# Kernel tuning notes

Measured on AMD Instinct MI355X. Metric: run time of the kernel, lower is better.

Reference implementation:

```python
import jax, jax.numpy as jnp
import numpy as np

N, E, H, XD, ED, YD, L = 10000, 640000, 128, 8, 8, 112, 4
EPS_MSG = 1e-7   # GENConv message eps
EPS_SM = 1e-16   # pyg softmax denom eps
EPS_LN = 1e-5    # layernorm eps


def node_ln(x, g, b):
    # torch.nn.LayerNorm over last dim
    m = x.mean(axis=-1, keepdims=True)
    v = x.var(axis=-1, keepdims=True)
    return (x - m) * jax.lax.rsqrt(v + EPS_LN) * g + b


def graph_ln(x, g, b):
    # pyg LayerNorm mode='graph' (no batch): global mean/std over all nodes+channels
    xc = x - x.mean()
    std = jnp.sqrt((xc * xc).mean())
    return xc / (std + EPS_LN) * g + b


def setup_inputs() -> dict:
    key = jax.random.key(0)
    ks = jax.random.split(key, 10)
    rn = lambda k, s, sc: jax.random.normal(k, s, jnp.float32) * sc
    return {
        "x": jax.random.normal(ks[0], (N, XD), jnp.float32),
        "edge_index": jax.random.randint(ks[1], (2, E), 0, N),
        "edge_attr": jax.random.normal(ks[2], (E, ED), jnp.float32),
        "Wn": rn(ks[3], (XD, H), 0.3), "bn": jnp.zeros((H,), jnp.float32),
        "We": rn(ks[4], (ED, H), 0.3), "be": jnp.zeros((H,), jnp.float32),
        "t": jnp.ones((L,), jnp.float32),
        "W1": rn(ks[5], (L, H, 2 * H), 0.08), "b1": jnp.zeros((L, 2 * H), jnp.float32),
        "g1": jnp.ones((L, 2 * H), jnp.float32), "bt1": jnp.zeros((L, 2 * H), jnp.float32),
        "W2": rn(ks[6], (L, 2 * H, H), 0.08), "b2": jnp.zeros((L, H), jnp.float32),
        "lng": jnp.ones((L, H), jnp.float32), "lnb": jnp.zeros((L, H), jnp.float32),
        "Wout": rn(ks[7], (H, YD), 0.08), "bout": jnp.zeros((YD,), jnp.float32),
    }


def reference(x, edge_index, edge_attr, Wn, bn, We, be, t, W1, b1, g1, bt1,
              W2, b2, lng, lnb, Wout, bout):
    src, dst = edge_index[0], edge_index[1]
    h = x @ Wn + bn                       # [N,H] node encoder
    ea = edge_attr @ We + be              # [E,H] edge encoder

    def gen_conv(h, i):
        msg = jax.nn.relu(h[src] + ea) + EPS_MSG          # [E,H]
        logit = msg * t[i]
        mx = jax.ops.segment_max(logit, dst, num_segments=N)
        ex = jnp.exp(logit - mx[dst])
        den = jax.ops.segment_sum(ex, dst, num_segments=N)
        alpha = ex / (den[dst] + EPS_SM)
        agg = jax.ops.segment_sum(alpha * msg, dst, num_segments=N) + h  # root add
        z = jax.nn.relu(graph_ln(agg @ W1[i] + b1[i], g1[i], bt1[i]))
        return z @ W2[i] + b2[i]

    h = gen_conv(h, 0)                    # first layer: conv only
    for i in range(1, L):                 # res+ blocks (dropout off: eval)
        r = jax.nn.relu(node_ln(h, lng[i], lnb[i]))
        h = h + gen_conv(r, i)
    h = jax.nn.relu(node_ln(h, lng[0], lnb[0]))  # layers[0].act(layers[0].norm(x))
    return h @ Wout + bout
```

## Files before the change

### kernel.cpp

```cpp
#include <hip/hip_runtime.h>
#include <math.h>

#define NN 10000
#define NE 640000
#define H 128
#define H2 256
#define XD 8
#define ED 8
#define YD 112
#define NL 4
#define EPS_MSG 1e-7f
#define EPS_SM 1e-16f
#define EPS_LN 1e-5f
#define TM 8
#define NB1 (NN / TM)
#define TNO 16
#define NBO (NN / TNO)

typedef _Float16 h2 __attribute__((ext_vector_type(2)));

__global__ void hist_k(const int* __restrict__ dst, int* __restrict__ counts) {
    int e = blockIdx.x * 256 + threadIdx.x;
    if (e < NE) atomicAdd(&counts[dst[e]], 1);
}

__global__ void scan_k(const int* __restrict__ counts, int* __restrict__ rowptr) {
    __shared__ int part[1024];
    int tid = threadIdx.x;
    const int CH = (NN + 1023) / 1024;
    int base = tid * CH;
    int s = 0;
    for (int j = 0; j < CH; j++) { int i = base + j; if (i < NN) s += counts[i]; }
    part[tid] = s; __syncthreads();
    for (int off = 1; off < 1024; off <<= 1) {
        int v = (tid >= off) ? part[tid - off] : 0;
        __syncthreads();
        part[tid] += v;
        __syncthreads();
    }
    int run = part[tid] - s;
    for (int j = 0; j < CH; j++) {
        int i = base + j;
        if (i < NN) { rowptr[i] = run; run += counts[i]; }
    }
    if (tid == 1023) rowptr[NN] = run;
}

__global__ void scatter_k(const int* __restrict__ dst, const int* __restrict__ rowptr,
                          int* __restrict__ fill, int* __restrict__ perm) {
    int e = blockIdx.x * 256 + threadIdx.x;
    if (e >= NE) return;
    int d = dst[e];
    int pos = rowptr[d] + atomicAdd(&fill[d], 1);
    perm[pos] = e;
}

__global__ void __launch_bounds__(256) packenc_k(
    const int* __restrict__ perm, const int* __restrict__ src,
    const float* __restrict__ eattr, int* __restrict__ srcs,
    _Float16* __restrict__ eacsr,
    const float* __restrict__ x, const float* __restrict__ Wn,
    const float* __restrict__ bn, float* __restrict__ h,
    _Float16* __restrict__ rh16) {
    int b = blockIdx.x;
    if (b < 2500) {
        int pos = b * 256 + threadIdx.x;
        int e = perm[pos];
        srcs[pos] = src[e];
        const float4* ein = (const float4*)eattr;
        float4 a = ein[(size_t)e * 2];
        float4 bb = ein[(size_t)e * 2 + 1];
        float4 pk;
        _Float16* pp = (_Float16*)&pk;
        pp[0] = (_Float16)a.x; pp[1] = (_Float16)a.y; pp[2] = (_Float16)a.z; pp[3] = (_Float16)a.w;
        pp[4] = (_Float16)bb.x; pp[5] = (_Float16)bb.y; pp[6] = (_Float16)bb.z; pp[7] = (_Float16)bb.w;
        ((float4*)eacsr)[pos] = pk;
    } else {
        int bb = b - 2500;
        int c = threadIdx.x & 127, ln = threadIdx.x >> 7;
        int n = bb * 2 + ln;
        const float4* xr = (const float4*)(x + (size_t)n * XD);
        float4 x0 = xr[0], x1 = xr[1];
        float acc = bn[c];
        acc = fmaf(x0.x, Wn[0 * H + c], acc); acc = fmaf(x0.y, Wn[1 * H + c], acc);
        acc = fmaf(x0.z, Wn[2 * H + c], acc); acc = fmaf(x0.w, Wn[3 * H + c], acc);
        acc = fmaf(x1.x, Wn[4 * H + c], acc); acc = fmaf(x1.y, Wn[5 * H + c], acc);
        acc = fmaf(x1.z, Wn[6 * H + c], acc); acc = fmaf(x1.w, Wn[7 * H + c], acc);
        h[(size_t)n * H + c] = acc;
        rh16[(size_t)n * H + c] = (_Float16)acc;
    }
}

__global__ void __launch_bounds__(512) ea_mm1_k(
    const float* __restrict__ rin, const _Float16* __restrict__ rh16,
    const int* __restrict__ rowptr,
    const int* __restrict__ srcs, const _Float16* __restrict__ eacsr,
    const float* __restrict__ We, const float* __restrict__ be,
    const float* __restrict__ tptr, int layer,
    const float* __restrict__ W1i, const float* __restrict__ b1i,
    float* __restrict__ y1, float* __restrict__ part) {
    int nb = blockIdx.x, tid = threadIdx.x;
    int n0 = nb * TM;
    __shared__ float a[TM][H];

    {
        int wv = tid >> 6, l = tid & 63;
        int c0 = 2 * l;
        int n = n0 + wv;
        h2 wA[4], wB[4];
#pragma unroll
        for (int k = 0; k < 4; k++) {
            wA[k][0] = (_Float16)We[(2 * k) * H + c0];
            wA[k][1] = (_Float16)We[(2 * k + 1) * H + c0];
            wB[k][0] = (_Float16)We[(2 * k) * H + c0 + 1];
            wB[k][1] = (_Float16)We[(2 * k + 1) * H + c0 + 1];
        }
        float becA = be[c0], becB = be[c0 + 1];
        float ts2 = tptr[layer] * 1.44269504088896f;
        int beg = __builtin_amdgcn_readfirstlane(rowptr[n]);
        int end = __builtin_amdgcn_readfirstlane(rowptr[n + 1]);
        const float2 rv = *(const float2*)(rin + (size_t)n * H + c0);
        float denA = 0.f, numA = 0.f, denB = 0.f, numB = 0.f;
#pragma unroll 4
        for (int j = beg; j < end; ++j) {
            int sn = srcs[j];
            float4 raw = *(const float4*)(eacsr + (size_t)j * ED);
            const h2* ep = (const h2*)&raw;
            h2 hv2 = *(const h2*)(rh16 + (size_t)sn * H + c0);
            float hvA = (float)hv2[0], hvB = (float)hv2[1];
            float pA = __builtin_amdgcn_fdot2(ep[0], wA[0], becA, false);
            pA = __builtin_amdgcn_fdot2(ep[1], wA[1], pA, false);
            pA = __builtin_amdgcn_fdot2(ep[2], wA[2], pA, false);
            pA = __builtin_amdgcn_fdot2(ep[3], wA[3], pA, false);
            float pB = __builtin_amdgcn_fdot2(ep[0], wB[0], becB, false);
            pB = __builtin_amdgcn_fdot2(ep[1], wB[1], pB, false);
            pB = __builtin_amdgcn_fdot2(ep[2], wB[2], pB, false);
            pB = __builtin_amdgcn_fdot2(ep[3], wB[3], pB, false);
            float msgA = fmaxf(hvA + pA, 0.f) + EPS_MSG;
            float msgB = fmaxf(hvB + pB, 0.f) + EPS_MSG;
            float peA = __builtin_amdgcn_exp2f(msgA * ts2);
            float peB = __builtin_amdgcn_exp2f(msgB * ts2);
            denA += peA; numA = fmaf(peA, msgA, numA);
            denB += peB; numB = fmaf(peB, msgB, numB);
        }
        float2 av;
        av.x = numA / (denA + EPS_SM) + rv.x;
        av.y = numB / (denB + EPS_SM) + rv.y;
        *(float2*)&a[wv][c0] = av;
    }
    __syncthreads();

    int o = tid & 255, half = tid >> 8;
    int rb = half * 4;
    float acc[4];
#pragma unroll
    for (int i = 0; i < 4; i++) acc[i] = 0.f;
    for (int k = 0; k < H; k += 4) {
        float w0 = W1i[k * H2 + o];
        float w1 = W1i[(k + 1) * H2 + o];
        float w2 = W1i[(k + 2) * H2 + o];
        float w3 = W1i[(k + 3) * H2 + o];
#pragma unroll
        for (int i = 0; i < 4; i++) {
            float4 av = *(const float4*)&a[rb + i][k];
            acc[i] = fmaf(av.x, w0, acc[i]);
            acc[i] = fmaf(av.y, w1, acc[i]);
            acc[i] = fmaf(av.z, w2, acc[i]);
            acc[i] = fmaf(av.w, w3, acc[i]);
        }
    }
    float bo = b1i[o];
    float ps = 0.f, ps2 = 0.f;
#pragma unroll
    for (int i = 0; i < 4; i++) {
        float v = acc[i] + bo;
        y1[(size_t)(n0 + rb + i) * H2 + o] = v;
        ps += v; ps2 += v * v;
    }
#pragma unroll
    for (int off = 32; off; off >>= 1) { ps += __shfl_xor(ps, off); ps2 += __shfl_xor(ps2, off); }
    __shared__ float red[16];
    int w8 = tid >> 6;
    if ((tid & 63) == 0) { red[w8] = ps; red[8 + w8] = ps2; }
    __syncthreads();
    if (tid == 0) {
        float S = 0.f, S2 = 0.f;
#pragma unroll
        for (int i = 0; i < 8; i++) { S += red[i]; S2 += red[8 + i]; }
        part[nb * 2] = S;
        part[nb * 2 + 1] = S2;
    }
}

__global__ void __launch_bounds__(256) mm2_k(const float* __restrict__ y1,
    const float* __restrict__ g1i, const float* __restrict__ bt1i,
    const float* __restrict__ W2i, const float* __restrict__ b2i,
    const float* __restrict__ part, float* __restrict__ h,
    const float* __restrict__ lgp, const float* __restrict__ lbp,
    float* __restrict__ r, _Float16* __restrict__ rh16, int first) {
    int nb = blockIdx.x, tid = threadIdx.x;
    int o = tid & 127, half = tid >> 7;
    int rb = half * 4;
    int n0 = nb * TM;
    float s = 0.f, s2 = 0.f;
    for (int i = tid; i < NB1; i += 256) { s += part[2 * i]; s2 += part[2 * i + 1]; }
#pragma unroll
    for (int off = 32; off; off >>= 1) { s += __shfl_xor(s, off); s2 += __shfl_xor(s2, off); }
    __shared__ float sred[8];
    int w4 = tid >> 6;
    if ((tid & 63) == 0) { sred[w4] = s; sred[4 + w4] = s2; }
    __syncthreads();
    const float M = (float)NN * (float)H2;
    float m = (sred[0] + sred[1] + sred[2] + sred[3]) / M;
    float var = fmaxf((sred[4] + sred[5] + sred[6] + sred[7]) / M - m * m, 0.f);
    float istd = 1.f / (sqrtf(var) + EPS_LN);

    __shared__ float z[TM][H2];
    __syncthreads();
    {
        const float4* y4 = (const float4*)(y1 + (size_t)n0 * H2);
        const float4* g4 = (const float4*)g1i;
        const float4* b4 = (const float4*)bt1i;
        float4* z4 = (float4*)z;
#pragma unroll
        for (int t = tid; t < TM * H2 / 4; t += 256) {
            int k4 = t & 63;
            float4 v = y4[t];
            float4 g = g4[k4], b = b4[k4];
            v.x = fmaxf((v.x - m) * istd * g.x + b.x, 0.f);
            v.y = fmaxf((v.y - m) * istd * g.y + b.y, 0.f);
            v.z = fmaxf((v.z - m) * istd * g.z + b.z, 0.f);
            v.w = fmaxf((v.w - m) * istd * g.w + b.w, 0.f);
            z4[t] = v;
        }
    }
    __syncthreads();
    float acc[4];
#pragma unroll
    for (int i = 0; i < 4; i++) acc[i] = 0.f;
    for (int k = 0; k < H2; k += 4) {
        float w0 = W2i[k * H + o];
        float w1 = W2i[(k + 1) * H + o];
        float w2 = W2i[(k + 2) * H + o];
        float w3 = W2i[(k + 3) * H + o];
#pragma unroll
        for (int i = 0; i < 4; i++) {
            float4 zv = *(const float4*)&z[rb + i][k];
            acc[i] = fmaf(zv.x, w0, acc[i]);
            acc[i] = fmaf(zv.y, w1, acc[i]);
            acc[i] = fmaf(zv.z, w2, acc[i]);
            acc[i] = fmaf(zv.w, w3, acc[i]);
        }
    }
    float bo = b2i[o];
    float vv[4];
#pragma unroll
    for (int i = 0; i < 4; i++) {
        size_t idx = (size_t)(n0 + rb + i) * H + o;
        float v = acc[i] + bo;
        if (!first) v += h[idx];
        h[idx] = v;
        vv[i] = v;
    }
    __shared__ float rs[2][2][4], rs2[2][2][4];
    int w2i_ = (tid >> 6) & 1;
#pragma unroll
    for (int i = 0; i < 4; i++) {
        float ss = vv[i], ss2 = vv[i] * vv[i];
#pragma unroll
        for (int off = 32; off; off >>= 1) { ss += __shfl_xor(ss, off); ss2 += __shfl_xor(ss2, off); }
        if ((tid & 63) == 0) { rs[half][w2i_][i] = ss; rs2[half][w2i_][i] = ss2; }
    }
    __syncthreads();
    float gc = lgp[o], bc = lbp[o];
#pragma unroll
    for (int i = 0; i < 4; i++) {
        float S = rs[half][0][i] + rs[half][1][i];
        float S2 = rs2[half][0][i] + rs2[half][1][i];
        float mn = S * (1.f / H);
        float vr = S2 * (1.f / H) - mn * mn;
        float inv = rsqrtf(vr + EPS_LN);
        float ov = fmaxf((vv[i] - mn) * inv * gc + bc, 0.f);
        size_t idx = (size_t)(n0 + rb + i) * H + o;
        r[idx] = ov;
        rh16[idx] = (_Float16)ov;
    }
}

__global__ void __launch_bounds__(128) mmout_k(const float* __restrict__ r,
    const float* __restrict__ Wout, const float* __restrict__ bout,
    float* __restrict__ out) {
    int nb = blockIdx.x, o = threadIdx.x;
    int n0 = nb * TNO;
    __shared__ float a[TNO][H];
    {
        const float4* r4 = (const float4*)(r + (size_t)n0 * H);
        float4* a4 = (float4*)a;
        for (int t = o; t < TNO * H / 4; t += 128) a4[t] = r4[t];
    }
    __syncthreads();
    if (o < YD) {
        float acc[TNO];
#pragma unroll
        for (int i = 0; i < TNO; i++) acc[i] = 0.f;
        for (int k = 0; k < H; k += 4) {
            float w0 = Wout[k * YD + o];
            float w1 = Wout[(k + 1) * YD + o];
            float w2 = Wout[(k + 2) * YD + o];
            float w3 = Wout[(k + 3) * YD + o];
#pragma unroll
            for (int i = 0; i < TNO; i++) {
                float4 av = *(const float4*)&a[i][k];
                acc[i] = fmaf(av.x, w0, acc[i]);
                acc[i] = fmaf(av.y, w1, acc[i]);
                acc[i] = fmaf(av.z, w2, acc[i]);
                acc[i] = fmaf(av.w, w3, acc[i]);
            }
        }
        float bo = bout[o];
#pragma unroll
        for (int i = 0; i < TNO; i++) out[(size_t)(n0 + i) * YD + o] = acc[i] + bo;
    }
}

extern "C" void kernel_launch(void* const* d_in, const int* in_sizes, int n_in,
                              void* d_out, int out_size, void* d_ws, size_t ws_size,
                              hipStream_t stream) {
    const float* x    = (const float*)d_in[0];
    const int*   ei   = (const int*)d_in[1];
    const float* eattr= (const float*)d_in[2];
    const float* Wn   = (const float*)d_in[3];
    const float* bn   = (const float*)d_in[4];
    const float* We   = (const float*)d_in[5];
    const float* be   = (const float*)d_in[6];
    const float* t    = (const float*)d_in[7];
    const float* W1   = (const float*)d_in[8];
    const float* b1   = (const float*)d_in[9];
    const float* g1   = (const float*)d_in[10];
    const float* bt1  = (const float*)d_in[11];
    const float* W2   = (const float*)d_in[12];
    const float* b2   = (const float*)d_in[13];
    const float* lng  = (const float*)d_in[14];
    const float* lnb  = (const float*)d_in[15];
    const float* Wout = (const float*)d_in[16];
    const float* bout = (const float*)d_in[17];
    float* out = (float*)d_out;

    const int* src = ei;
    const int* dst = ei + NE;

    char* ws = (char*)d_ws;
    size_t off = 0;
    auto alloc = [&](size_t bytes) -> char* {
        char* p = ws + off;
        off += (bytes + 255) & ~(size_t)255;
        return p;
    };
    int*      counts = (int*)alloc((size_t)NN * 2 * 4);
    int*      fill   = counts + NN;
    int*      rowptr = (int*)alloc((size_t)(NN + 1) * 4);
    int*      perm   = (int*)alloc((size_t)NE * 4);
    int*      srcs   = (int*)alloc((size_t)NE * 4);
    _Float16* eacsr  = (_Float16*)alloc((size_t)NE * ED * 2);
    float*    h      = (float*)alloc((size_t)NN * H * 4);
    float*    r      = (float*)alloc((size_t)NN * H * 4);
    _Float16* rh16   = (_Float16*)alloc((size_t)NN * H * 2);
    float*    y1     = (float*)alloc((size_t)NN * H2 * 4);
    float*    part   = (float*)alloc((size_t)NB1 * 2 * 4);
    (void)ws_size; (void)in_sizes; (void)n_in; (void)out_size;

    hipMemsetAsync(counts, 0, (size_t)NN * 2 * 4, stream);

    hist_k<<<(NE + 255) / 256, 256, 0, stream>>>(dst, counts);
    scan_k<<<1, 1024, 0, stream>>>(counts, rowptr);
    scatter_k<<<(NE + 255) / 256, 256, 0, stream>>>(dst, rowptr, fill, perm);
    packenc_k<<<2500 + NN / 2, 256, 0, stream>>>(perm, src, eattr, srcs, eacsr,
                                                 x, Wn, bn, h, rh16);

    for (int i = 0; i < NL; i++) {
        const float* cin = (i == 0) ? h : r;
        ea_mm1_k<<<NB1, 512, 0, stream>>>(cin, rh16, rowptr, srcs, eacsr, We, be, t, i,
                                          W1 + (size_t)i * H * H2, b1 + i * H2, y1, part);
        int nx = (i == NL - 1) ? 0 : (i + 1);
        mm2_k<<<NB1, 256, 0, stream>>>(y1, g1 + i * H2, bt1 + i * H2,
                                       W2 + (size_t)i * H2 * H, b2 + i * H, part, h,
                                       lng + nx * H, lnb + nx * H, r, rh16, (i == 0) ? 1 : 0);
    }
    mmout_k<<<NBO, 128, 0, stream>>>(r, Wout, bout, out);
}
```

Before: 473.9 us.

## Split edge aggregation into edge-balanced kernel with atomic segment accumulation

Replaces the per-node CSR aggregation loop, where one wave handles all edges of one node, with an edge-parallel kernel. Each wave takes a fixed tile of 64 sorted edges and flushes partial softmax denominators and numerators to global buffers with float atomics whenever the destination changes. A separate kernel then divides and adds the root before mm1, and the buffers are re-zeroed in mm2. This is meant to remove load imbalance from uneven node degrees, at the cost of an extra kernel launch, extra global traffic for the den/num buffers, and atomic contention.

```diff
diff --git a/kernel.cpp b/kernel.cpp
--- a/kernel.cpp
+++ b/kernel.cpp
@@ -12,6 +12,8 @@
 #define EPS_MSG 1e-7f
 #define EPS_SM 1e-16f
 #define EPS_LN 1e-5f
+#define ETILE 64
+#define NEB (NE / (ETILE * 4))
 #define TM 8
 #define NB1 (NN / TM)
 #define TNO 16
@@ -57,16 +59,17 @@
 
 __global__ void __launch_bounds__(256) packenc_k(
     const int* __restrict__ perm, const int* __restrict__ src,
-    const float* __restrict__ eattr, int* __restrict__ srcs,
-    _Float16* __restrict__ eacsr,
+    const int* __restrict__ dstf, const float* __restrict__ eattr,
+    int* __restrict__ srcs, int* __restrict__ dstp, _Float16* __restrict__ eacsr,
     const float* __restrict__ x, const float* __restrict__ Wn,
     const float* __restrict__ bn, float* __restrict__ h,
-    _Float16* __restrict__ rh16) {
+    _Float16* __restrict__ rh16, float* __restrict__ deng, float* __restrict__ numg) {
     int b = blockIdx.x;
     if (b < 2500) {
         int pos = b * 256 + threadIdx.x;
         int e = perm[pos];
         srcs[pos] = src[e];
+        dstp[pos] = dstf[e];
         const float4* ein = (const float4*)eattr;
         float4 a = ein[(size_t)e * 2];
         float4 bb = ein[(size_t)e * 2 + 1];
@@ -86,67 +89,84 @@
         acc = fmaf(x0.z, Wn[2 * H + c], acc); acc = fmaf(x0.w, Wn[3 * H + c], acc);
         acc = fmaf(x1.x, Wn[4 * H + c], acc); acc = fmaf(x1.y, Wn[5 * H + c], acc);
         acc = fmaf(x1.z, Wn[6 * H + c], acc); acc = fmaf(x1.w, Wn[7 * H + c], acc);
-        h[(size_t)n * H + c] = acc;
-        rh16[(size_t)n * H + c] = (_Float16)acc;
-    }
-}
-
-__global__ void __launch_bounds__(512) ea_mm1_k(
-    const float* __restrict__ rin, const _Float16* __restrict__ rh16,
-    const int* __restrict__ rowptr,
+        size_t idx = (size_t)n * H + c;
+        h[idx] = acc;
+        rh16[idx] = (_Float16)acc;
+        deng[idx] = 0.f;
+        numg[idx] = 0.f;
+    }
+}
+
+__global__ void __launch_bounds__(256) edge_k(
+    const _Float16* __restrict__ rh16, const int* __restrict__ dstp,
     const int* __restrict__ srcs, const _Float16* __restrict__ eacsr,
     const float* __restrict__ We, const float* __restrict__ be,
     const float* __restrict__ tptr, int layer,
+    float* __restrict__ deng, float* __restrict__ numg) {
+    int tid = threadIdx.x;
+    int wv = tid >> 6, l = tid & 63;
+    int c0 = 2 * l;
+    int j0 = (blockIdx.x * 4 + wv) * ETILE;
+
+    h2 wA[4], wB[4];
+#pragma unroll
+    for (int k = 0; k < 4; k++) {
+        wA[k][0] = (_Float16)We[(2 * k) * H + c0];
+        wA[k][1] = (_Float16)We[(2 * k + 1) * H + c0];
+        wB[k][0] = (_Float16)We[(2 * k) * H + c0 + 1];
+        wB[k][1] = (_Float16)We[(2 * k + 1) * H + c0 + 1];
+    }
+    float becA = be[c0], becB = be[c0 + 1];
+    float ts2 = tptr[layer] * 1.44269504088896f;
+
+    int cur = __builtin_amdgcn_readfirstlane(dstp[j0]);
+    float denA = 0.f, numA = 0.f, denB = 0.f, numB = 0.f;
+#pragma unroll 4
+    for (int j = j0; j < j0 + ETILE; ++j) {
+        int d = __builtin_amdgcn_readfirstlane(dstp[j]);
+        if (d != cur) {
+            size_t bi = (size_t)cur * H + c0;
+            atomicAdd(&deng[bi], denA);     atomicAdd(&deng[bi + 1], denB);
+            atomicAdd(&numg[bi], numA);     atomicAdd(&numg[bi + 1], numB);
+            denA = 0.f; numA = 0.f; denB = 0.f; numB = 0.f;
+            cur = d;
+        }
+        int sn = srcs[j];
+        float4 raw = *(const float4*)(eacsr + (size_t)j * ED);
+        const h2* ep = (const h2*)&raw;
+        h2 hv2 = *(const h2*)(rh16 + (size_t)sn * H + c0);
+        float hvA = (float)hv2[0], hvB = (float)hv2[1];
+        float pA = __builtin_amdgcn_fdot2(ep[0], wA[0], becA, false);
+        pA = __builtin_amdgcn_fdot2(ep[1], wA[1], pA, false);
+        pA = __builtin_amdgcn_fdot2(ep[2], wA[2], pA, false);
+        pA = __builtin_amdgcn_fdot2(ep[3], wA[3], pA, false);
+        float pB = __builtin_amdgcn_fdot2(ep[0], wB[0], becB, false);
+        pB = __builtin_amdgcn_fdot2(ep[1], wB[1], pB, false);
+        pB = __builtin_amdgcn_fdot2(ep[2], wB[2], pB, false);
+        pB = __builtin_amdgcn_fdot2(ep[3], wB[3], pB, false);
+        float msgA = fmaxf(hvA + pA, 0.f) + EPS_MSG;
+        float msgB = fmaxf(hvB + pB, 0.f) + EPS_MSG;
+        float peA = __builtin_amdgcn_exp2f(msgA * ts2);
+        float peB = __builtin_amdgcn_exp2f(msgB * ts2);
+        denA += peA; numA = fmaf(peA, msgA, numA);
+        denB += peB; numB = fmaf(peB, msgB, numB);
+    }
+    size_t bi = (size_t)cur * H + c0;
+    atomicAdd(&deng[bi], denA);     atomicAdd(&deng[bi + 1], denB);
+    atomicAdd(&numg[bi], numA);     atomicAdd(&numg[bi + 1], numB);
+}
+
+__global__ void __launch_bounds__(512) fin_mm1_k(
+    const float* __restrict__ rin,
+    const float* __restrict__ deng, const float* __restrict__ numg,
     const float* __restrict__ W1i, const float* __restrict__ b1i,
     float* __restrict__ y1, float* __restrict__ part) {
     int nb = blockIdx.x, tid = threadIdx.x;
     int n0 = nb * TM;
     __shared__ float a[TM][H];
-
-    {
-        int wv = tid >> 6, l = tid & 63;
-        int c0 = 2 * l;
-        int n = n0 + wv;
-        h2 wA[4], wB[4];
-#pragma unroll
-        for (int k = 0; k < 4; k++) {
-            wA[k][0] = (_Float16)We[(2 * k) * H + c0];
-            wA[k][1] = (_Float16)We[(2 * k + 1) * H + c0];
-            wB[k][0] = (_Float16)We[(2 * k) * H + c0 + 1];
-            wB[k][1] = (_Float16)We[(2 * k + 1) * H + c0 + 1];
-        }
-        float becA = be[c0], becB = be[c0 + 1];
-        float ts2 = tptr[layer] * 1.44269504088896f;
-        int beg = __builtin_amdgcn_readfirstlane(rowptr[n]);
-        int end = __builtin_amdgcn_readfirstlane(rowptr[n + 1]);
-        const float2 rv = *(const float2*)(rin + (size_t)n * H + c0);
-        float denA = 0.f, numA = 0.f, denB = 0.f, numB = 0.f;
-#pragma unroll 4
-        for (int j = beg; j < end; ++j) {
-            int sn = srcs[j];
-            float4 raw = *(const float4*)(eacsr + (size_t)j * ED);
-            const h2* ep = (const h2*)&raw;
-            h2 hv2 = *(const h2*)(rh16 + (size_t)sn * H + c0);
-            float hvA = (float)hv2[0], hvB = (float)hv2[1];
-            float pA = __builtin_amdgcn_fdot2(ep[0], wA[0], becA, false);
-            pA = __builtin_amdgcn_fdot2(ep[1], wA[1], pA, false);
-            pA = __builtin_amdgcn_fdot2(ep[2], wA[2], pA, false);
-            pA = __builtin_amdgcn_fdot2(ep[3], wA[3], pA, false);
-            float pB = __builtin_amdgcn_fdot2(ep[0], wB[0], becB, false);
-            pB = __builtin_amdgcn_fdot2(ep[1], wB[1], pB, false);
-            pB = __builtin_amdgcn_fdot2(ep[2], wB[2], pB, false);
-            pB = __builtin_amdgcn_fdot2(ep[3], wB[3], pB, false);
-            float msgA = fmaxf(hvA + pA, 0.f) + EPS_MSG;
-            float msgB = fmaxf(hvB + pB, 0.f) + EPS_MSG;
-            float peA = __builtin_amdgcn_exp2f(msgA * ts2);
-            float peB = __builtin_amdgcn_exp2f(msgB * ts2);
-            denA += peA; numA = fmaf(peA, msgA, numA);
-            denB += peB; numB = fmaf(peB, msgB, numB);
-        }
-        float2 av;
-        av.x = numA / (denA + EPS_SM) + rv.x;
-        av.y = numB / (denB + EPS_SM) + rv.y;
-        *(float2*)&a[wv][c0] = av;
+    for (int t = tid; t < TM * H; t += 512) {
+        size_t idx = (size_t)n0 * H + t;
+        ((float*)a)[t] = numg[idx] / (deng[idx] + EPS_SM) + rin[idx];
     }
     __syncthreads();
 
@@ -197,7 +217,8 @@
     const float* __restrict__ W2i, const float* __restrict__ b2i,
     const float* __restrict__ part, float* __restrict__ h,
     const float* __restrict__ lgp, const float* __restrict__ lbp,
-    float* __restrict__ r, _Float16* __restrict__ rh16, int first) {
+    float* __restrict__ r, _Float16* __restrict__ rh16,
+    float* __restrict__ deng, float* __restrict__ numg, int first) {
     int nb = blockIdx.x, tid = threadIdx.x;
     int o = tid & 127, half = tid >> 7;
     int rb = half * 4;
@@ -284,6 +305,8 @@
         size_t idx = (size_t)(n0 + rb + i) * H + o;
         r[idx] = ov;
         rh16[idx] = (_Float16)ov;
+        deng[idx] = 0.f;
+        numg[idx] = 0.f;
     }
 }
 
@@ -361,10 +384,13 @@
     int*      rowptr = (int*)alloc((size_t)(NN + 1) * 4);
     int*      perm   = (int*)alloc((size_t)NE * 4);
     int*      srcs   = (int*)alloc((size_t)NE * 4);
+    int*      dstp   = (int*)alloc((size_t)NE * 4);
     _Float16* eacsr  = (_Float16*)alloc((size_t)NE * ED * 2);
     float*    h      = (float*)alloc((size_t)NN * H * 4);
     float*    r      = (float*)alloc((size_t)NN * H * 4);
     _Float16* rh16   = (_Float16*)alloc((size_t)NN * H * 2);
+    float*    deng   = (float*)alloc((size_t)NN * H * 4);
+    float*    numg   = (float*)alloc((size_t)NN * H * 4);
     float*    y1     = (float*)alloc((size_t)NN * H2 * 4);
     float*    part   = (float*)alloc((size_t)NB1 * 2 * 4);
     (void)ws_size; (void)in_sizes; (void)n_in; (void)out_size;
@@ -374,17 +400,20 @@
     hist_k<<<(NE + 255) / 256, 256, 0, stream>>>(dst, counts);
     scan_k<<<1, 1024, 0, stream>>>(counts, rowptr);
     scatter_k<<<(NE + 255) / 256, 256, 0, stream>>>(dst, rowptr, fill, perm);
-    packenc_k<<<2500 + NN / 2, 256, 0, stream>>>(perm, src, eattr, srcs, eacsr,
-                                                 x, Wn, bn, h, rh16);
+    packenc_k<<<2500 + NN / 2, 256, 0, stream>>>(perm, src, dst, eattr, srcs, dstp,
+                                                 eacsr, x, Wn, bn, h, rh16, deng, numg);
 
     for (int i = 0; i < NL; i++) {
         const float* cin = (i == 0) ? h : r;
-        ea_mm1_k<<<NB1, 512, 0, stream>>>(cin, rh16, rowptr, srcs, eacsr, We, be, t, i,
-                                          W1 + (size_t)i * H * H2, b1 + i * H2, y1, part);
+        edge_k<<<NEB, 256, 0, stream>>>(rh16, dstp, srcs, eacsr, We, be, t, i,
+                                        deng, numg);
+        fin_mm1_k<<<NB1, 512, 0, stream>>>(cin, deng, numg,
+                                           W1 + (size_t)i * H * H2, b1 + i * H2, y1, part);
         int nx = (i == NL - 1) ? 0 : (i + 1);
         mm2_k<<<NB1, 256, 0, stream>>>(y1, g1 + i * H2, bt1 + i * H2,
                                        W2 + (size_t)i * H2 * H, b2 + i * H, part, h,
-                                       lng + nx * H, lnb + nx * H, r, rh16, (i == 0) ? 1 : 0);
+                                       lng + nx * H, lnb + nx * H, r, rh16,
+                                       deng, numg, (i == 0) ? 1 : 0);
     }
     mmout_k<<<NBO, 128, 0, stream>>>(r, Wout, bout, out);
 }
```

Measured after the change: 712.4 us. 50.3% more time.

## Bucket nodes by in-degree so each aggregation block processes similar-degree nodes

Applied to the files above, without the earlier changes.

Computes a degree histogram during the scan and builds a node ordering grouped by in-degree buckets. The aggregation+mm1 kernel then assigns each block's 8 waves to nodes from this ordering instead of consecutive node ids. This aims to cut idle time where waves wait at the block barrier for the highest-degree node. It adds a small bucketing pass and makes per-node row accesses and y1 stores non-contiguous.

```diff
diff --git a/kernel.cpp b/kernel.cpp
--- a/kernel.cpp
+++ b/kernel.cpp
@@ -16,6 +16,7 @@
 #define NB1 (NN / TM)
 #define TNO 16
 #define NBO (NN / TNO)
+#define NBK 32
 
 typedef _Float16 h2 __attribute__((ext_vector_type(2)));
 
@@ -24,13 +25,22 @@
     if (e < NE) atomicAdd(&counts[dst[e]], 1);
 }
 
-__global__ void scan_k(const int* __restrict__ counts, int* __restrict__ rowptr) {
+__global__ void scan_k(const int* __restrict__ counts, int* __restrict__ rowptr,
+                       int* __restrict__ bucketStart) {
     __shared__ int part[1024];
+    __shared__ int bh[NBK];
     int tid = threadIdx.x;
+    if (tid < NBK) bh[tid] = 0;
     const int CH = (NN + 1023) / 1024;
     int base = tid * CH;
     int s = 0;
-    for (int j = 0; j < CH; j++) { int i = base + j; if (i < NN) s += counts[i]; }
+    for (int j = 0; j < CH; j++) {
+        int i = base + j;
+        if (i < NN) {
+            int d = counts[i];
+            s += d;
+        }
+    }
     part[tid] = s; __syncthreads();
     for (int off = 1; off < 1024; off <<= 1) {
         int v = (tid >= off) ? part[tid - off] : 0;
@@ -41,18 +51,39 @@
     int run = part[tid] - s;
     for (int j = 0; j < CH; j++) {
         int i = base + j;
-        if (i < NN) { rowptr[i] = run; run += counts[i]; }
+        if (i < NN) {
+            int d = counts[i];
+            rowptr[i] = run; run += d;
+            atomicAdd(&bh[min(d >> 3, NBK - 1)], 1);
+        }
     }
     if (tid == 1023) rowptr[NN] = run;
+    __syncthreads();
+    if (tid == 0) {
+        int acc = 0;
+        for (int b = 0; b < NBK; b++) { bucketStart[b] = acc; acc += bh[b]; }
+    }
 }
 
 __global__ void scatter_k(const int* __restrict__ dst, const int* __restrict__ rowptr,
-                          int* __restrict__ fill, int* __restrict__ perm) {
-    int e = blockIdx.x * 256 + threadIdx.x;
-    if (e >= NE) return;
-    int d = dst[e];
-    int pos = rowptr[d] + atomicAdd(&fill[d], 1);
-    perm[pos] = e;
+                          int* __restrict__ fill, int* __restrict__ perm,
+                          const int* __restrict__ bucketStart, int* __restrict__ bfill,
+                          int* __restrict__ nodeorder) {
+    int b = blockIdx.x;
+    if (b < 2500) {
+        int e = b * 256 + threadIdx.x;
+        int d = dst[e];
+        int pos = rowptr[d] + atomicAdd(&fill[d], 1);
+        perm[pos] = e;
+    } else {
+        int n = (b - 2500) * 256 + threadIdx.x;
+        if (n < NN) {
+            int deg = rowptr[n + 1] - rowptr[n];
+            int bk = min(deg >> 3, NBK - 1);
+            int pos = bucketStart[bk] + atomicAdd(&bfill[bk], 1);
+            nodeorder[pos] = n;
+        }
+    }
 }
 
 __global__ void __launch_bounds__(256) packenc_k(
@@ -93,7 +124,7 @@
 
 __global__ void __launch_bounds__(512) ea_mm1_k(
     const float* __restrict__ rin, const _Float16* __restrict__ rh16,
-    const int* __restrict__ rowptr,
+    const int* __restrict__ rowptr, const int* __restrict__ nodeorder,
     const int* __restrict__ srcs, const _Float16* __restrict__ eacsr,
     const float* __restrict__ We, const float* __restrict__ be,
     const float* __restrict__ tptr, int layer,
@@ -102,11 +133,14 @@
     int nb = blockIdx.x, tid = threadIdx.x;
     int n0 = nb * TM;
     __shared__ float a[TM][H];
+    __shared__ int nodes_s[TM];
+    if (tid < TM) nodes_s[tid] = nodeorder[n0 + tid];
+    __syncthreads();
 
     {
         int wv = tid >> 6, l = tid & 63;
         int c0 = 2 * l;
-        int n = n0 + wv;
+        int n = nodes_s[wv];
         h2 wA[4], wB[4];
 #pragma unroll
         for (int k = 0; k < 4; k++) {
@@ -174,7 +208,7 @@
 #pragma unroll
     for (int i = 0; i < 4; i++) {
         float v = acc[i] + bo;
-        y1[(size_t)(n0 + rb + i) * H2 + o] = v;
+        y1[(size_t)nodes_s[rb + i] * H2 + o] = v;
         ps += v; ps2 += v * v;
     }
 #pragma unroll
@@ -356,10 +390,13 @@
         off += (bytes + 255) & ~(size_t)255;
         return p;
     };
-    int*      counts = (int*)alloc((size_t)NN * 2 * 4);
+    int*      counts = (int*)alloc((size_t)(NN * 2 + NBK) * 4);
     int*      fill   = counts + NN;
+    int*      bfill  = counts + 2 * NN;
+    int*      bucketStart = (int*)alloc((size_t)NBK * 4);
     int*      rowptr = (int*)alloc((size_t)(NN + 1) * 4);
     int*      perm   = (int*)alloc((size_t)NE * 4);
+    int*      nodeorder = (int*)alloc((size_t)NN * 4);
     int*      srcs   = (int*)alloc((size_t)NE * 4);
     _Float16* eacsr  = (_Float16*)alloc((size_t)NE * ED * 2);
     float*    h      = (float*)alloc((size_t)NN * H * 4);
@@ -369,17 +406,19 @@
     float*    part   = (float*)alloc((size_t)NB1 * 2 * 4);
     (void)ws_size; (void)in_sizes; (void)n_in; (void)out_size;
 
-    hipMemsetAsync(counts, 0, (size_t)NN * 2 * 4, stream);
+    hipMemsetAsync(counts, 0, (size_t)(NN * 2 + NBK) * 4, stream);
 
     hist_k<<<(NE + 255) / 256, 256, 0, stream>>>(dst, counts);
-    scan_k<<<1, 1024, 0, stream>>>(counts, rowptr);
-    scatter_k<<<(NE + 255) / 256, 256, 0, stream>>>(dst, rowptr, fill, perm);
+    scan_k<<<1, 1024, 0, stream>>>(counts, rowptr, bucketStart);
+    scatter_k<<<2500 + (NN + 255) / 256, 256, 0, stream>>>(dst, rowptr, fill, perm,
+                                                           bucketStart, bfill, nodeorder);
     packenc_k<<<2500 + NN / 2, 256, 0, stream>>>(perm, src, eattr, srcs, eacsr,
                                                  x, Wn, bn, h, rh16);
 
     for (int i = 0; i < NL; i++) {
         const float* cin = (i == 0) ? h : r;
-        ea_mm1_k<<<NB1, 512, 0, stream>>>(cin, rh16, rowptr, srcs, eacsr, We, be, t, i,
+        ea_mm1_k<<<NB1, 512, 0, stream>>>(cin, rh16, rowptr, nodeorder, srcs, eacsr,
+                                          We, be, t, i,
                                           W1 + (size_t)i * H * H2, b1 + i * H2, y1, part);
         int nx = (i == NL - 1) ? 0 : (i + 1);
         mm2_k<<<NB1, 256, 0, stream>>>(y1, g1 + i * H2, bt1 + i * H2,
```

New measurement: 522.7 us. +10.3%, slower.

## Group nodes by in-degree bucket so each aggregation block gets balanced work

Applied to the files above, without the earlier changes.

The scan kernel now buckets nodes by in-degree (degree/8, 32 buckets) and writes a node order sorted by bucket. The fused aggregation+mm1 kernel assigns each block's 8 waves to nodes drawn from that order, so the waves in a block have similar edge counts and fewer sit idle waiting on the longest one. Output rows of y1 are written to the permuted node indices. This adds a small amount of atomic work in the single-block scan and scattered y1 row writes, and the bounds check in scatter_k is dropped because NE is divisible by 256.

```diff
diff --git a/kernel.cpp b/kernel.cpp
--- a/kernel.cpp
+++ b/kernel.cpp
@@ -16,6 +16,7 @@
 #define NB1 (NN / TM)
 #define TNO 16
 #define NBO (NN / TNO)
+#define NBK 32
 
 typedef _Float16 h2 __attribute__((ext_vector_type(2)));
 
@@ -24,14 +25,31 @@
     if (e < NE) atomicAdd(&counts[dst[e]], 1);
 }
 
-__global__ void scan_k(const int* __restrict__ counts, int* __restrict__ rowptr) {
+__global__ void scan_k(const int* __restrict__ counts, int* __restrict__ rowptr,
+                       int* __restrict__ nodeorder) {
     __shared__ int part[1024];
+    __shared__ int bstart[NBK];
+    __shared__ int bfill[NBK];
     int tid = threadIdx.x;
+    if (tid < NBK) { bstart[tid] = 0; bfill[tid] = 0; }
+    __syncthreads();
     const int CH = (NN + 1023) / 1024;
     int base = tid * CH;
+    int degs[CH];
     int s = 0;
-    for (int j = 0; j < CH; j++) { int i = base + j; if (i < NN) s += counts[i]; }
-    part[tid] = s; __syncthreads();
+#pragma unroll
+    for (int j = 0; j < CH; j++) {
+        int i = base + j;
+        degs[j] = (i < NN) ? counts[i] : 0;
+        s += degs[j];
+    }
+    part[tid] = s;
+#pragma unroll
+    for (int j = 0; j < CH; j++) {
+        int i = base + j;
+        if (i < NN) atomicAdd(&bstart[min(degs[j] >> 3, NBK - 1)], 1);
+    }
+    __syncthreads();
     for (int off = 1; off < 1024; off <<= 1) {
         int v = (tid >= off) ? part[tid - off] : 0;
         __syncthreads();
@@ -39,17 +57,32 @@
         __syncthreads();
     }
     int run = part[tid] - s;
+#pragma unroll
     for (int j = 0; j < CH; j++) {
         int i = base + j;
-        if (i < NN) { rowptr[i] = run; run += counts[i]; }
+        if (i < NN) { rowptr[i] = run; run += degs[j]; }
     }
     if (tid == 1023) rowptr[NN] = run;
+    __syncthreads();
+    if (tid == 0) {
+        int acc = 0;
+        for (int b = 0; b < NBK; b++) { int c = bstart[b]; bstart[b] = acc; acc += c; }
+    }
+    __syncthreads();
+#pragma unroll
+    for (int j = 0; j < CH; j++) {
+        int i = base + j;
+        if (i < NN) {
+            int bk = min(degs[j] >> 3, NBK - 1);
+            int pos = bstart[bk] + atomicAdd(&bfill[bk], 1);
+            nodeorder[pos] = i;
+        }
+    }
 }
 
 __global__ void scatter_k(const int* __restrict__ dst, const int* __restrict__ rowptr,
                           int* __restrict__ fill, int* __restrict__ perm) {
     int e = blockIdx.x * 256 + threadIdx.x;
-    if (e >= NE) return;
     int d = dst[e];
     int pos = rowptr[d] + atomicAdd(&fill[d], 1);
     perm[pos] = e;
@@ -93,7 +126,7 @@
 
 __global__ void __launch_bounds__(512) ea_mm1_k(
     const float* __restrict__ rin, const _Float16* __restrict__ rh16,
-    const int* __restrict__ rowptr,
+    const int* __restrict__ rowptr, const int* __restrict__ nodeorder,
     const int* __restrict__ srcs, const _Float16* __restrict__ eacsr,
     const float* __restrict__ We, const float* __restrict__ be,
     const float* __restrict__ tptr, int layer,
@@ -102,11 +135,14 @@
     int nb = blockIdx.x, tid = threadIdx.x;
     int n0 = nb * TM;
     __shared__ float a[TM][H];
+    __shared__ int nodes_s[TM];
+    if (tid < TM) nodes_s[tid] = nodeorder[n0 + tid];
+    __syncthreads();
 
     {
         int wv = tid >> 6, l = tid & 63;
         int c0 = 2 * l;
-        int n = n0 + wv;
+        int n = nodes_s[wv];
         h2 wA[4], wB[4];
 #pragma unroll
         for (int k = 0; k < 4; k++) {
@@ -174,7 +210,7 @@
 #pragma unroll
     for (int i = 0; i < 4; i++) {
         float v = acc[i] + bo;
-        y1[(size_t)(n0 + rb + i) * H2 + o] = v;
+        y1[(size_t)nodes_s[rb + i] * H2 + o] = v;
         ps += v; ps2 += v * v;
     }
 #pragma unroll
@@ -360,6 +396,7 @@
     int*      fill   = counts + NN;
     int*      rowptr = (int*)alloc((size_t)(NN + 1) * 4);
     int*      perm   = (int*)alloc((size_t)NE * 4);
+    int*      nodeorder = (int*)alloc((size_t)NN * 4);
     int*      srcs   = (int*)alloc((size_t)NE * 4);
     _Float16* eacsr  = (_Float16*)alloc((size_t)NE * ED * 2);
     float*    h      = (float*)alloc((size_t)NN * H * 4);
@@ -372,14 +409,15 @@
     hipMemsetAsync(counts, 0, (size_t)NN * 2 * 4, stream);
 
     hist_k<<<(NE + 255) / 256, 256, 0, stream>>>(dst, counts);
-    scan_k<<<1, 1024, 0, stream>>>(counts, rowptr);
-    scatter_k<<<(NE + 255) / 256, 256, 0, stream>>>(dst, rowptr, fill, perm);
+    scan_k<<<1, 1024, 0, stream>>>(counts, rowptr, nodeorder);
+    scatter_k<<<NE / 256, 256, 0, stream>>>(dst, rowptr, fill, perm);
     packenc_k<<<2500 + NN / 2, 256, 0, stream>>>(perm, src, eattr, srcs, eacsr,
                                                  x, Wn, bn, h, rh16);
 
     for (int i = 0; i < NL; i++) {
         const float* cin = (i == 0) ? h : r;
-        ea_mm1_k<<<NB1, 512, 0, stream>>>(cin, rh16, rowptr, srcs, eacsr, We, be, t, i,
+        ea_mm1_k<<<NB1, 512, 0, stream>>>(cin, rh16, rowptr, nodeorder, srcs, eacsr,
+                                          We, be, t, i,
                                           W1 + (size_t)i * H * H2, b1 + i * H2, y1, part);
         int nx = (i == NL - 1) ? 0 : (i + 1);
         mm2_k<<<NB1, 256, 0, stream>>>(y1, g1 + i * H2, bt1 + i * H2,
```

Result: no change. 479.1 us (+1.1%).
